# Performance work log

Hardware: AMD Instinct MI355X
Metric: run time of the kernel (lower is better)

The kernel has to match this reference:

```python
import jax, jax.numpy as jnp
import numpy as np
import math

ALPHA = 1.3
N_ITER = 50


def entmax_bisect(logits, alpha=ALPHA, n_iter=N_ITER):
    # logits: [..., D]; entmax over the last axis via bisection on tau.
    x = logits / max(1.0, abs(alpha - 1.0))  # divisor is 1.0 for alpha=1.3
    x = x - jnp.max(x, axis=-1, keepdims=True)  # max_x subtraction (differentiable, as in torch)
    xs = jax.lax.stop_gradient(x)  # tau_lo/tau_hi are .detach()'d in the original
    tau_lo = jnp.min(xs, axis=-1, keepdims=True) - 1.0
    tau_hi = jnp.max(xs, axis=-1, keepdims=True) - 1e-6
    inv = 1.0 / (alpha - 1.0)

    def body(_, carry):
        lo, hi = carry
        tau = (lo + hi) * 0.5
        p = jnp.maximum(xs - tau, 0.0) ** inv
        f = jnp.sum(p, axis=-1, keepdims=True) ** (alpha - 1.0)
        big = f > 1.0
        return (jnp.where(big, tau, lo), jnp.where(big, hi, tau))

    tau_lo, tau_hi = jax.lax.fori_loop(0, n_iter, body, (tau_lo, tau_hi))
    tau = (tau_lo + tau_hi) * 0.5
    p = jnp.maximum(x - tau, 0.0) ** inv
    return p / (jnp.sum(p, axis=-1, keepdims=True) + 1e-12)


def setup_inputs() -> dict:
    key = jax.random.key(0)
    kq, kk, kv = jax.random.split(key, 3)
    B, N, D = 16, 2048, 64
    return {
        "q": jax.random.normal(kq, (B, N, D), dtype=jnp.float32),
        "k": jax.random.normal(kk, (B, N, D), dtype=jnp.float32),
        "v": jax.random.normal(kv, (B, N, D), dtype=jnp.float32),
    }


def reference(q, k, v):
    d = q.shape[-1]
    scores = jnp.einsum("bnd,bmd->bnm", q, k) / math.sqrt(d)  # [B,N,N]
    attn = entmax_bisect(scores, alpha=ALPHA)
    out = jnp.einsum("bnm,bmd->bnd", attn, v)
    return out, attn
```

## Files before the change

### kernel.cpp

```cpp
#include <hip/hip_runtime.h>


#define NBATCH 16
#define NSEQ   2048
#define DHEAD  64
#define OUT_OFF (NBATCH * NSEQ * DHEAD)
#define INV_A    3.3333333f
#define INV_A_M1 2.3333333f

typedef float  vfloat4 __attribute__((ext_vector_type(4)));
typedef float  f32x4   __attribute__((ext_vector_type(4)));
typedef short  bf16x8  __attribute__((ext_vector_type(8)));
typedef unsigned short u16x8 __attribute__((ext_vector_type(8)));

__device__ __forceinline__ float fast_log2(float x) { return __builtin_amdgcn_logf(x); }
__device__ __forceinline__ float fast_exp2(float x) { return __builtin_amdgcn_exp2f(x); }

__device__ __forceinline__ unsigned bf16_rne(float x) {
    const unsigned u = __float_as_uint(x);
    return (u + 0x7FFFu + ((u >> 16) & 1u)) >> 16;
}

__global__ __launch_bounds__(256) void ksplit_kernel(
    const float* __restrict__ K, unsigned short* __restrict__ Khi,
    unsigned short* __restrict__ Klo)
{
    const size_t idx = (size_t)blockIdx.x * 256 + threadIdx.x;
    const float4 x = ((const float4*)K)[idx];
    const float xs[4] = {x.x, x.y, x.z, x.w};
    unsigned short h[4], l[4];
    #pragma unroll
    for (int i = 0; i < 4; ++i) {
        const unsigned hr = bf16_rne(xs[i]);
        h[i] = (unsigned short)hr;
        l[i] = (unsigned short)bf16_rne(xs[i] - __uint_as_float(hr << 16));
    }
    ((ushort4*)Khi)[idx] = make_ushort4(h[0], h[1], h[2], h[3]);
    ((ushort4*)Klo)[idx] = make_ushort4(l[0], l[1], l[2], l[3]);
}

__global__ __launch_bounds__(512, 4) void entmax_attn_kernel(
    const float* __restrict__ Q, const float* __restrict__ V,
    float* __restrict__ Out,
    const unsigned short* __restrict__ Khi, const unsigned short* __restrict__ Klo)
{
    __shared__ __align__(16) float reg0[8192];
    __shared__ __align__(16) float cvx[8 * 512];

    const int tid  = threadIdx.x;
    const int w    = tid >> 6;
    const int lane = tid & 63;
    const int arow = lane & 15;
    const int lg   = lane >> 4;

    const int i   = blockIdx.x;
    const int xcd = i & 7;
    const int j2  = i >> 3;
    const int b   = xcd + 8 * (j2 & 1);
    const int rb  = j2 >> 1;
    const int n0  = rb * 16;

    const float* Vb = V + (size_t)b * NSEQ * DHEAD;
    const unsigned short* KhiB = Khi + (size_t)b * NSEQ * DHEAD;
    const unsigned short* KloB = Klo + (size_t)b * NSEQ * DHEAD;
    char* ldsHi = (char*)reg0;
    char* ldsLo = (char*)reg0 + 16384;

    bf16x8 a_hi[2], a_lo[2];
    {
        const float* qrow = Q + ((size_t)b * NSEQ + (size_t)(n0 + arow)) * DHEAD;
        #pragma unroll
        for (int ks = 0; ks < 2; ++ks) {
            const int d0 = ks * 32 + lg * 8;
            const float4 x0 = *(const float4*)(qrow + d0);
            const float4 x1 = *(const float4*)(qrow + d0 + 4);
            const float xs[8] = {x0.x, x0.y, x0.z, x0.w, x1.x, x1.y, x1.z, x1.w};
            #pragma unroll
            for (int e = 0; e < 8; ++e) {
                const float xq = xs[e] * 0.125f;
                const unsigned hr = bf16_rne(xq);
                a_hi[ks][e] = (short)hr;
                a_lo[ks][e] = (short)bf16_rne(xq - __uint_as_float(hr << 16));
            }
        }
    }

    float s[2][32];
    const int kap = 16 * w + arow;

    const int keyA = tid >> 3, cA = tid & 7;
    const int keyB = keyA + 64;
    const size_t gA = (size_t)keyA * DHEAD + cA * 8;
    const size_t gB = (size_t)keyB * DHEAD + cA * 8;
    const int ofA = keyA * 128 + ((cA ^ (keyA & 7)) << 4);
    const int ofB = keyB * 128 + ((cA ^ (keyA & 7)) << 4);

    u16x8 shA = *(const u16x8*)(KhiB + gA), slA = *(const u16x8*)(KloB + gA);
    u16x8 shB = *(const u16x8*)(KhiB + gB), slB = *(const u16x8*)(KloB + gB);

    #pragma unroll
    for (int g = 0; g < 4; ++g) {
        f32x4 acc[4];
        #pragma unroll
        for (int tt = 0; tt < 4; ++tt) acc[tt] = (f32x4){0.f, 0.f, 0.f, 0.f};

        #pragma unroll
        for (int tt = 0; tt < 4; ++tt) {
            const int t = 4 * g + tt;
            __syncthreads();
            *(u16x8*)(ldsHi + ofA) = shA;  *(u16x8*)(ldsLo + ofA) = slA;
            *(u16x8*)(ldsHi + ofB) = shB;  *(u16x8*)(ldsLo + ofB) = slB;
            __syncthreads();

            #pragma unroll
            for (int ks = 0; ks < 2; ++ks) {
                const int loff = kap * 128 + ((((ks << 2) | lg) ^ (kap & 7)) << 4);
                const bf16x8 bh = *(const bf16x8*)(ldsHi + loff);
                const bf16x8 bl = *(const bf16x8*)(ldsLo + loff);
                acc[tt] = __builtin_amdgcn_mfma_f32_16x16x32_bf16(a_hi[ks], bh, acc[tt], 0, 0, 0);
                acc[tt] = __builtin_amdgcn_mfma_f32_16x16x32_bf16(a_hi[ks], bl, acc[tt], 0, 0, 0);
                acc[tt] = __builtin_amdgcn_mfma_f32_16x16x32_bf16(a_lo[ks], bh, acc[tt], 0, 0, 0);
            }
            if (t < 15) {
                const size_t tb = (size_t)(t + 1) * (128 * DHEAD);
                shA = *(const u16x8*)(KhiB + tb + gA);
                slA = *(const u16x8*)(KloB + tb + gA);
                shB = *(const u16x8*)(KhiB + tb + gB);
                slB = *(const u16x8*)(KloB + tb + gB);
            }
        }

        __syncthreads();
        #pragma unroll
        for (int tt = 0; tt < 4; ++tt)
            #pragma unroll
            for (int i2 = 0; i2 < 4; ++i2)
                reg0[(lg * 4 + i2) * 512 + tt * 128 + kap] = acc[tt][i2];
        __syncthreads();
        #pragma unroll
        for (int r = 0; r < 2; ++r)
            #pragma unroll
            for (int jj = 0; jj < 8; ++jj)
                s[r][8 * g + jj] = reg0[(2 * w + r) * 512 + jj * 64 + lane];
    }
    __syncthreads();

    float* prow  = reg0 + w * 1024;
    float* cval0 = cvx + w * 512;
    float* cidx0 = cval0 + 128;
    float* cval1 = cval0 + 256;
    float* cidx1 = cval0 + 384;
    const unsigned long long lt_mask = (1ull << lane) - 1ull;
    const int na = n0 + 2 * w;

    float mx0 = s[0][0], mx1 = s[1][0];
    #pragma unroll
    for (int j = 1; j < 32; ++j) { mx0 = fmaxf(mx0, s[0][j]); mx1 = fmaxf(mx1, s[1][j]); }
    #pragma unroll
    for (int off = 32; off >= 1; off >>= 1) {
        mx0 = fmaxf(mx0, __shfl_xor(mx0, off, 64));
        mx1 = fmaxf(mx1, __shfl_xor(mx1, off, 64));
    }
    #pragma unroll
    for (int j = 0; j < 32; ++j) { s[0][j] -= mx0; s[1][j] -= mx1; }

    int base0 = 0, base1 = 0;
    #pragma unroll
    for (int j = 0; j < 32; ++j) {
        const bool a0 = s[0][j] > -1.0f;
        const bool a1 = s[1][j] > -1.0f;
        const unsigned long long bm0 = __ballot(a0);
        const unsigned long long bm1 = __ballot(a1);
        const int q0 = base0 + __popcll(bm0 & lt_mask);
        const int q1 = base1 + __popcll(bm1 & lt_mask);
        if (a0 && q0 < 128) { cval0[q0] = s[0][j]; cidx0[q0] = (float)(j * 64 + lane); }
        if (a1 && q1 < 128) { cval1[q1] = s[1][j]; cidx1[q1] = (float)(j * 64 + lane); }
        base0 += __popcll(bm0);
        base1 += __popcll(bm1);
    }
    const int A0 = base0, A1 = base1;

    float* arow0 = Out + OUT_OFF + ((size_t)b * NSEQ + na) * NSEQ;
    float* arow1 = arow0 + NSEQ;

    if (A0 <= 128 && A1 <= 128) {
        const float cv00 = cval0[lane], cv01 = cval0[64 + lane];
        const float cv10 = cval1[lane], cv11 = cval1[64 + lane];
        const bool ok00 = lane < A0, ok01 = 64 + lane < A0;
        const bool ok10 = lane < A1, ok11 = 64 + lane < A1;

        float lo0 = -1.0f, hi0 = -1e-6f, lo1 = -1.0f, hi1 = -1e-6f;
        #pragma unroll 1
        for (int it = 0; it < 12; ++it) {
            const float ta = 0.5f * (lo0 + hi0);
            const float tb = 0.5f * (lo1 + hi1);
            const float t00 = cv00 - ta, t01 = cv01 - ta;
            const float t10 = cv10 - tb, t11 = cv11 - tb;
            float S0 = ((ok00 && t00 > 0.f) ? fast_exp2(INV_A * fast_log2(t00)) : 0.f)
                     + ((ok01 && t01 > 0.f) ? fast_exp2(INV_A * fast_log2(t01)) : 0.f);
            float S1 = ((ok10 && t10 > 0.f) ? fast_exp2(INV_A * fast_log2(t10)) : 0.f)
                     + ((ok11 && t11 > 0.f) ? fast_exp2(INV_A * fast_log2(t11)) : 0.f);
            #pragma unroll
            for (int off = 32; off >= 1; off >>= 1) {
                S0 += __shfl_xor(S0, off, 64);
                S1 += __shfl_xor(S1, off, 64);
            }
            if (S0 > 1.f) lo0 = ta; else hi0 = ta;
            if (S1 > 1.f) lo1 = tb; else hi1 = tb;
        }
        float tau0 = lo0, tau1 = lo1;
        #pragma unroll 1
        for (int it = 0; it < 2; ++it) {
            const float t00 = cv00 - tau0, t01 = cv01 - tau0;
            const float t10 = cv10 - tau1, t11 = cv11 - tau1;
            float Sa0 = 0.f, Sb0 = 0.f, Sa1 = 0.f, Sb1 = 0.f;
            if (ok00 && t00 > 0.f) { const float l = fast_log2(t00); Sa0 += fast_exp2(INV_A * l); Sb0 += fast_exp2(INV_A_M1 * l); }
            if (ok01 && t01 > 0.f) { const float l = fast_log2(t01); Sa0 += fast_exp2(INV_A * l); Sb0 += fast_exp2(INV_A_M1 * l); }
            if (ok10 && t10 > 0.f) { const float l = fast_log2(t10); Sa1 += fast_exp2(INV_A * l); Sb1 += fast_exp2(INV_A_M1 * l); }
            if (ok11 && t11 > 0.f) { const float l = fast_log2(t11); Sa1 += fast_exp2(INV_A * l); Sb1 += fast_exp2(INV_A_M1 * l); }
            #pragma unroll
            for (int off = 32; off >= 1; off >>= 1) {
                Sa0 += __shfl_xor(Sa0, off, 64); Sb0 += __shfl_xor(Sb0, off, 64);
                Sa1 += __shfl_xor(Sa1, off, 64); Sb1 += __shfl_xor(Sb1, off, 64);
            }
            tau0 += (Sa0 - 1.f) / (INV_A * Sb0);
            tau0 = fmaxf(fminf(tau0, hi0), lo0);
            tau1 += (Sa1 - 1.f) / (INV_A * Sb1);
            tau1 = fmaxf(fminf(tau1, hi1), lo1);
        }

        const float t00 = cv00 - tau0, t01 = cv01 - tau0;
        const float t10 = cv10 - tau1, t11 = cv11 - tau1;
        float p00 = (ok00 && t00 > 0.f) ? fast_exp2(INV_A * fast_log2(t00)) : 0.f;
        float p01 = (ok01 && t01 > 0.f) ? fast_exp2(INV_A * fast_log2(t01)) : 0.f;
        float p10 = (ok10 && t10 > 0.f) ? fast_exp2(INV_A * fast_log2(t10)) : 0.f;
        float p11 = (ok11 && t11 > 0.f) ? fast_exp2(INV_A * fast_log2(t11)) : 0.f;
        float S0 = p00 + p01, S1 = p10 + p11;
        #pragma unroll
        for (int off = 32; off >= 1; off >>= 1) {
            S0 += __shfl_xor(S0, off, 64);
            S1 += __shfl_xor(S1, off, 64);
        }
        const float rn0 = 1.f / (S0 + 1e-12f);
        const float rn1 = 1.f / (S1 + 1e-12f);
        p00 *= rn0; p01 *= rn0; p10 *= rn1; p11 *= rn1;
        const int i00 = ok00 ? (int)cidx0[lane] : 0;
        const int i01 = ok01 ? (int)cidx0[64 + lane] : 0;
        const int i10 = ok10 ? (int)cidx1[lane] : 0;
        const int i11 = ok11 ? (int)cidx1[64 + lane] : 0;
        if (ok00) cval0[lane] = p00;
        if (ok01) cval0[64 + lane] = p01;
        if (ok10) cval1[lane] = p10;
        if (ok11) cval1[64 + lane] = p11;

        #pragma unroll
        for (int seg = 0; seg < 2; ++seg) {
            #pragma unroll
            for (int z = 0; z < 4; ++z)
                *(float4*)&prow[(z * 64 + lane) * 4] = make_float4(0.f, 0.f, 0.f, 0.f);
            if (ok00 && (i00 >> 10) == seg) prow[i00 & 1023] = p00;
            if (ok01 && (i01 >> 10) == seg) prow[i01 & 1023] = p01;
            #pragma unroll
            for (int z = 0; z < 4; ++z) {
                const vfloat4 pv = *(const vfloat4*)&prow[(z * 64 + lane) * 4];
                __builtin_nontemporal_store(pv,
                    (vfloat4*)&arow0[seg * 1024 + (z * 64 + lane) * 4]);
            }
        }
        #pragma unroll
        for (int seg = 0; seg < 2; ++seg) {
            #pragma unroll
            for (int z = 0; z < 4; ++z)
                *(float4*)&prow[(z * 64 + lane) * 4] = make_float4(0.f, 0.f, 0.f, 0.f);
            if (ok10 && (i10 >> 10) == seg) prow[i10 & 1023] = p10;
            if (ok11 && (i11 >> 10) == seg) prow[i11 & 1023] = p11;
            #pragma unroll
            for (int z = 0; z < 4; ++z) {
                const vfloat4 pv = *(const vfloat4*)&prow[(z * 64 + lane) * 4];
                __builtin_nontemporal_store(pv,
                    (vfloat4*)&arow1[seg * 1024 + (z * 64 + lane) * 4]);
            }
        }

        float out0 = 0.f, out1 = 0.f;
        int ii = 0;
        #pragma unroll 1
        for (; ii + 8 <= A0; ii += 8) {
            const float pa = cval0[ii+0], pb = cval0[ii+1], pc = cval0[ii+2], pd = cval0[ii+3];
            const float pe = cval0[ii+4], pf = cval0[ii+5], pg = cval0[ii+6], ph = cval0[ii+7];
            const int ma = (int)cidx0[ii+0], mb = (int)cidx0[ii+1], mc = (int)cidx0[ii+2], md = (int)cidx0[ii+3];
            const int me = (int)cidx0[ii+4], mf = (int)cidx0[ii+5], mg = (int)cidx0[ii+6], mh = (int)cidx0[ii+7];
            const float va = Vb[(size_t)ma * DHEAD + lane], vb2 = Vb[(size_t)mb * DHEAD + lane];
            const float vc = Vb[(size_t)mc * DHEAD + lane], vd  = Vb[(size_t)md * DHEAD + lane];
            const float ve = Vb[(size_t)me * DHEAD + lane], vf  = Vb[(size_t)mf * DHEAD + lane];
            const float vg = Vb[(size_t)mg * DHEAD + lane], vh  = Vb[(size_t)mh * DHEAD + lane];
            out0 += pa*va + pb*vb2 + pc*vc + pd*vd + pe*ve + pf*vf + pg*vg + ph*vh;
        }
        #pragma unroll 1
        for (; ii < A0; ++ii)
            out0 += cval0[ii] * Vb[(size_t)(int)cidx0[ii] * DHEAD + lane];

        int jj = 0;
        #pragma unroll 1
        for (; jj + 8 <= A1; jj += 8) {
            const float pa = cval1[jj+0], pb = cval1[jj+1], pc = cval1[jj+2], pd = cval1[jj+3];
            const float pe = cval1[jj+4], pf = cval1[jj+5], pg = cval1[jj+6], ph = cval1[jj+7];
            const int ma = (int)cidx1[jj+0], mb = (int)cidx1[jj+1], mc = (int)cidx1[jj+2], md = (int)cidx1[jj+3];
            const int me = (int)cidx1[jj+4], mf = (int)cidx1[jj+5], mg = (int)cidx1[jj+6], mh = (int)cidx1[jj+7];
            const float va = Vb[(size_t)ma * DHEAD + lane], vb2 = Vb[(size_t)mb * DHEAD + lane];
            const float vc = Vb[(size_t)mc * DHEAD + lane], vd  = Vb[(size_t)md * DHEAD + lane];
            const float ve = Vb[(size_t)me * DHEAD + lane], vf  = Vb[(size_t)mf * DHEAD + lane];
            const float vg = Vb[(size_t)mg * DHEAD + lane], vh  = Vb[(size_t)mh * DHEAD + lane];
            out1 += pa*va + pb*vb2 + pc*vc + pd*vd + pe*ve + pf*vf + pg*vg + ph*vh;
        }
        #pragma unroll 1
        for (; jj < A1; ++jj)
            out1 += cval1[jj] * Vb[(size_t)(int)cidx1[jj] * DHEAD + lane];

        Out[((size_t)b * NSEQ + na) * DHEAD + lane] = out0;
        Out[((size_t)b * NSEQ + na + 1) * DHEAD + lane] = out1;
    } else {
        #pragma unroll
        for (int r = 0; r < 2; ++r) {
            const int A = r ? A1 : A0;
            float* cval = r ? cval1 : cval0;
            float* cidx = r ? cidx1 : cidx0;
            float* arowX = r ? arow1 : arow0;
            float outacc = 0.f;

            if (A <= 128) {
                const float cv0 = cval[lane];
                const float cv1 = cval[64 + lane];
                const bool ok0 = (lane < A);
                const bool ok1 = (64 + lane < A);

                float lo = -1.0f, hi = -1e-6f;
                #pragma unroll 1
                for (int it = 0; it < 12; ++it) {
                    const float tau = 0.5f * (lo + hi);
                    const float t0 = cv0 - tau, t1 = cv1 - tau;
                    float S = ((ok0 && t0 > 0.f) ? fast_exp2(INV_A * fast_log2(t0)) : 0.f)
                            + ((ok1 && t1 > 0.f) ? fast_exp2(INV_A * fast_log2(t1)) : 0.f);
                    #pragma unroll
                    for (int off = 32; off >= 1; off >>= 1) S += __shfl_xor(S, off, 64);
                    if (S > 1.f) lo = tau; else hi = tau;
                }
                float tau = lo;
                #pragma unroll 1
                for (int it = 0; it < 2; ++it) {
                    const float t0 = cv0 - tau, t1 = cv1 - tau;
                    float S1 = 0.f, S2 = 0.f;
                    if (ok0 && t0 > 0.f) {
                        const float l = fast_log2(t0);
                        S1 += fast_exp2(INV_A * l); S2 += fast_exp2(INV_A_M1 * l);
                    }
                    if (ok1 && t1 > 0.f) {
                        const float l = fast_log2(t1);
                        S1 += fast_exp2(INV_A * l); S2 += fast_exp2(INV_A_M1 * l);
                    }
                    #pragma unroll
                    for (int off = 32; off >= 1; off >>= 1) {
                        S1 += __shfl_xor(S1, off, 64);
                        S2 += __shfl_xor(S2, off, 64);
                    }
                    tau += (S1 - 1.f) / (INV_A * S2);
                    tau = fmaxf(fminf(tau, hi), lo);
                }

                const float t0 = cv0 - tau, t1 = cv1 - tau;
                float p0 = (ok0 && t0 > 0.f) ? fast_exp2(INV_A * fast_log2(t0)) : 0.f;
                float p1 = (ok1 && t1 > 0.f) ? fast_exp2(INV_A * fast_log2(t1)) : 0.f;
                float S = p0 + p1;
                #pragma unroll
                for (int off = 32; off >= 1; off >>= 1) S += __shfl_xor(S, off, 64);
                const float rnorm = 1.f / (S + 1e-12f);
                p0 *= rnorm; p1 *= rnorm;
                const int i0 = ok0 ? (int)cidx[lane] : 0;
                const int i1 = ok1 ? (int)cidx[64 + lane] : 0;
                if (ok0) cval[lane] = p0;
                if (ok1) cval[64 + lane] = p1;

                #pragma unroll
                for (int seg = 0; seg < 2; ++seg) {
                    #pragma unroll
                    for (int z = 0; z < 4; ++z)
                        *(float4*)&prow[(z * 64 + lane) * 4] = make_float4(0.f, 0.f, 0.f, 0.f);
                    if (ok0 && (i0 >> 10) == seg) prow[i0 & 1023] = p0;
                    if (ok1 && (i1 >> 10) == seg) prow[i1 & 1023] = p1;
                    #pragma unroll
                    for (int z = 0; z < 4; ++z) {
                        const vfloat4 pv = *(const vfloat4*)&prow[(z * 64 + lane) * 4];
                        __builtin_nontemporal_store(pv,
                            (vfloat4*)&arowX[seg * 1024 + (z * 64 + lane) * 4]);
                    }
                }

                int ii = 0;
                #pragma unroll 1
                for (; ii + 4 <= A; ii += 4) {
                    const float pa = cval[ii + 0], pb = cval[ii + 1];
                    const float pc = cval[ii + 2], pd = cval[ii + 3];
                    const int ma = (int)cidx[ii + 0], mb = (int)cidx[ii + 1];
                    const int mc = (int)cidx[ii + 2], md = (int)cidx[ii + 3];
                    const float va = Vb[(size_t)ma * DHEAD + lane];
                    const float vb2 = Vb[(size_t)mb * DHEAD + lane];
                    const float vc = Vb[(size_t)mc * DHEAD + lane];
                    const float vd = Vb[(size_t)md * DHEAD + lane];
                    outacc += pa * va + pb * vb2 + pc * vc + pd * vd;
                }
                #pragma unroll 1
                for (; ii < A; ++ii)
                    outacc += cval[ii] * Vb[(size_t)(int)cidx[ii] * DHEAD + lane];
            } else {
                float lo = -1.0f, hi = -1e-6f;
                #pragma unroll 1
                for (int it = 0; it < 12; ++it) {
                    const float tau = 0.5f * (lo + hi);
                    float S = 0.f;
                    #pragma unroll
                    for (int j = 0; j < 32; ++j) {
                        const float t = s[r][j] - tau;
                        const float p = fast_exp2(INV_A * fast_log2(t));
                        S += (t > 0.f) ? p : 0.f;
                    }
                    #pragma unroll
                    for (int off = 32; off >= 1; off >>= 1) S += __shfl_xor(S, off, 64);
                    if (S > 1.f) lo = tau; else hi = tau;
                }
                float tau = lo;
                #pragma unroll 1
                for (int it = 0; it < 2; ++it) {
                    float S1 = 0.f, S2 = 0.f;
                    #pragma unroll
                    for (int j = 0; j < 32; ++j) {
                        const float t = s[r][j] - tau;
                        if (t > 0.f) {
                            const float l = fast_log2(t);
                            S1 += fast_exp2(INV_A * l); S2 += fast_exp2(INV_A_M1 * l);
                        }
                    }
                    #pragma unroll
                    for (int off = 32; off >= 1; off >>= 1) {
                        S1 += __shfl_xor(S1, off, 64);
                        S2 += __shfl_xor(S2, off, 64);
                    }
                    tau += (S1 - 1.f) / (INV_A * S2);
                    tau = fmaxf(fminf(tau, hi), lo);
                }
                float S = 0.f;
                #pragma unroll
                for (int j = 0; j < 32; ++j) {
                    const float t = s[r][j] - tau;
                    const float p = (t > 0.f) ? fast_exp2(INV_A * fast_log2(t)) : 0.f;
                    s[r][j] = p;
                    S += p;
                }
                #pragma unroll
                for (int off = 32; off >= 1; off >>= 1) S += __shfl_xor(S, off, 64);
                const float rnorm = 1.f / (S + 1e-12f);

                #pragma unroll
                for (int seg = 0; seg < 2; ++seg) {
                    #pragma unroll
                    for (int jj = 0; jj < 16; ++jj)
                        prow[jj * 64 + lane] = s[r][seg * 16 + jj] * rnorm;
                    #pragma unroll
                    for (int z = 0; z < 16; ++z)
                        __builtin_nontemporal_store(prow[z * 64 + lane],
                                                    &arowX[seg * 1024 + z * 64 + lane]);
                    #pragma unroll 4
                    for (int m = 0; m < 1024; ++m)
                        outacc += prow[m] * Vb[(size_t)(seg * 1024 + m) * DHEAD + lane];
                }
            }

            Out[((size_t)b * NSEQ + (na + r)) * DHEAD + lane] = outacc;
        }
    }
}

extern "C" void kernel_launch(void* const* d_in, const int* in_sizes, int n_in,
                              void* d_out, int out_size, void* d_ws, size_t ws_size,
                              hipStream_t stream) {
    const float* q = (const float*)d_in[0];
    const float* k = (const float*)d_in[1];
    const float* v = (const float*)d_in[2];
    float* out = (float*)d_out;
    (void)in_sizes; (void)n_in; (void)out_size; (void)ws_size;

    unsigned short* Khi = (unsigned short*)d_ws;
    unsigned short* Klo = Khi + (size_t)NBATCH * NSEQ * DHEAD;

    hipLaunchKernelGGL(ksplit_kernel, dim3(2048), dim3(256), 0, stream, k, Khi, Klo);
    hipLaunchKernelGGL(entmax_attn_kernel, dim3(2048), dim3(512), 0, stream,
                       q, v, out, Khi, Klo);
}
```

Before: 451.9 us.

## Pack candidate value and index into one word, cut bisection iterations, recompute dense fallback

Candidate logits and their column indices are packed into a single 32-bit word (value mantissa truncated, index in the low 11 bits), halving the shared-memory candidate buffer and the loads in the sparse gather loops. The number of bisection iterations before the Newton refinement drops from 12 to 8 or 10 on the sparse paths. The rare dense fallback now recomputes scores from fp32 K instead of keeping them live in registers, and uses shuffles instead of shared memory for the P·V product. This lowers register and LDS pressure. The costs are truncated precision on the stored values and probabilities, fewer bisection steps, and removal of the explicit occupancy hint from launch bounds.

Result: slower. 641.0 us (+41.8%).

```diff
diff --git a/kernel.cpp b/kernel.cpp
--- a/kernel.cpp
+++ b/kernel.cpp
@@ -7,6 +7,8 @@
 #define OUT_OFF (NBATCH * NSEQ * DHEAD)
 #define INV_A    3.3333333f
 #define INV_A_M1 2.3333333f
+#define IDXM 0x7FFu
+#define VALM 0xFFFFF800u
 
 typedef float  vfloat4 __attribute__((ext_vector_type(4)));
 typedef float  f32x4   __attribute__((ext_vector_type(4)));
@@ -39,13 +41,13 @@
     ((ushort4*)Klo)[idx] = make_ushort4(l[0], l[1], l[2], l[3]);
 }
 
-__global__ __launch_bounds__(512, 4) void entmax_attn_kernel(
-    const float* __restrict__ Q, const float* __restrict__ V,
-    float* __restrict__ Out,
+__global__ __launch_bounds__(512) void entmax_attn_kernel(
+    const float* __restrict__ Q, const float* __restrict__ K,
+    const float* __restrict__ V, float* __restrict__ Out,
     const unsigned short* __restrict__ Khi, const unsigned short* __restrict__ Klo)
 {
     __shared__ __align__(16) float reg0[8192];
-    __shared__ __align__(16) float cvx[8 * 512];
+    __shared__ __align__(16) float cpk[8 * 256];
 
     const int tid  = threadIdx.x;
     const int w    = tid >> 6;
@@ -60,6 +62,7 @@
     const int rb  = j2 >> 1;
     const int n0  = rb * 16;
 
+    const float* Kb = K + (size_t)b * NSEQ * DHEAD;
     const float* Vb = V + (size_t)b * NSEQ * DHEAD;
     const unsigned short* KhiB = Khi + (size_t)b * NSEQ * DHEAD;
     const unsigned short* KloB = Klo + (size_t)b * NSEQ * DHEAD;
@@ -145,11 +148,9 @@
     }
     __syncthreads();
 
-    float* prow  = reg0 + w * 1024;
-    float* cval0 = cvx + w * 512;
-    float* cidx0 = cval0 + 128;
-    float* cval1 = cval0 + 256;
-    float* cidx1 = cval0 + 384;
+    unsigned* pk0 = (unsigned*)(cpk + w * 256);
+    unsigned* pk1 = pk0 + 128;
+    float* prow = reg0 + w * 1024;
     const unsigned long long lt_mask = (1ull << lane) - 1ull;
     const int na = n0 + 2 * w;
 
@@ -161,20 +162,21 @@
         mx0 = fmaxf(mx0, __shfl_xor(mx0, off, 64));
         mx1 = fmaxf(mx1, __shfl_xor(mx1, off, 64));
     }
-    #pragma unroll
-    for (int j = 0; j < 32; ++j) { s[0][j] -= mx0; s[1][j] -= mx1; }
 
     int base0 = 0, base1 = 0;
     #pragma unroll
     for (int j = 0; j < 32; ++j) {
-        const bool a0 = s[0][j] > -1.0f;
-        const bool a1 = s[1][j] > -1.0f;
+        const float v0 = s[0][j] - mx0;
+        const float v1 = s[1][j] - mx1;
+        const bool a0 = v0 > -1.0f;
+        const bool a1 = v1 > -1.0f;
         const unsigned long long bm0 = __ballot(a0);
         const unsigned long long bm1 = __ballot(a1);
         const int q0 = base0 + __popcll(bm0 & lt_mask);
         const int q1 = base1 + __popcll(bm1 & lt_mask);
-        if (a0 && q0 < 128) { cval0[q0] = s[0][j]; cidx0[q0] = (float)(j * 64 + lane); }
-        if (a1 && q1 < 128) { cval1[q1] = s[1][j]; cidx1[q1] = (float)(j * 64 + lane); }
+        const unsigned idx = (unsigned)(j * 64 + lane);
+        if (a0 && q0 < 128) pk0[q0] = (__float_as_uint(v0) & VALM) | idx;
+        if (a1 && q1 < 128) pk1[q1] = (__float_as_uint(v1) & VALM) | idx;
         base0 += __popcll(bm0);
         base1 += __popcll(bm1);
     }
@@ -184,14 +186,18 @@
     float* arow1 = arow0 + NSEQ;
 
     if (A0 <= 128 && A1 <= 128) {
-        const float cv00 = cval0[lane], cv01 = cval0[64 + lane];
-        const float cv10 = cval1[lane], cv11 = cval1[64 + lane];
+        const unsigned u00 = pk0[lane],      u01 = pk0[64 + lane];
+        const unsigned u10 = pk1[lane],      u11 = pk1[64 + lane];
+        const float cv00 = __uint_as_float(u00 & VALM);
+        const float cv01 = __uint_as_float(u01 & VALM);
+        const float cv10 = __uint_as_float(u10 & VALM);
+        const float cv11 = __uint_as_float(u11 & VALM);
         const bool ok00 = lane < A0, ok01 = 64 + lane < A0;
         const bool ok10 = lane < A1, ok11 = 64 + lane < A1;
 
         float lo0 = -1.0f, hi0 = -1e-6f, lo1 = -1.0f, hi1 = -1e-6f;
         #pragma unroll 1
-        for (int it = 0; it < 12; ++it) {
+        for (int it = 0; it < 8; ++it) {
             const float ta = 0.5f * (lo0 + hi0);
             const float tb = 0.5f * (lo1 + hi1);
             const float t00 = cv00 - ta, t01 = cv01 - ta;
@@ -244,14 +250,14 @@
         const float rn0 = 1.f / (S0 + 1e-12f);
         const float rn1 = 1.f / (S1 + 1e-12f);
         p00 *= rn0; p01 *= rn0; p10 *= rn1; p11 *= rn1;
-        const int i00 = ok00 ? (int)cidx0[lane] : 0;
-        const int i01 = ok01 ? (int)cidx0[64 + lane] : 0;
-        const int i10 = ok10 ? (int)cidx1[lane] : 0;
-        const int i11 = ok11 ? (int)cidx1[64 + lane] : 0;
-        if (ok00) cval0[lane] = p00;
-        if (ok01) cval0[64 + lane] = p01;
-        if (ok10) cval1[lane] = p10;
-        if (ok11) cval1[64 + lane] = p11;
+        const int i00 = ok00 ? (int)(u00 & IDXM) : -1;
+        const int i01 = ok01 ? (int)(u01 & IDXM) : -1;
+        const int i10 = ok10 ? (int)(u10 & IDXM) : -1;
+        const int i11 = ok11 ? (int)(u11 & IDXM) : -1;
+        if (ok00) pk0[lane]      = (__float_as_uint(p00) & VALM) | (unsigned)i00;
+        if (ok01) pk0[64 + lane] = (__float_as_uint(p01) & VALM) | (unsigned)i01;
+        if (ok10) pk1[lane]      = (__float_as_uint(p10) & VALM) | (unsigned)i10;
+        if (ok11) pk1[64 + lane] = (__float_as_uint(p11) & VALM) | (unsigned)i11;
 
         #pragma unroll
         for (int seg = 0; seg < 2; ++seg) {
@@ -286,57 +292,62 @@
         int ii = 0;
         #pragma unroll 1
         for (; ii + 8 <= A0; ii += 8) {
-            const float pa = cval0[ii+0], pb = cval0[ii+1], pc = cval0[ii+2], pd = cval0[ii+3];
-            const float pe = cval0[ii+4], pf = cval0[ii+5], pg = cval0[ii+6], ph = cval0[ii+7];
-            const int ma = (int)cidx0[ii+0], mb = (int)cidx0[ii+1], mc = (int)cidx0[ii+2], md = (int)cidx0[ii+3];
-            const int me = (int)cidx0[ii+4], mf = (int)cidx0[ii+5], mg = (int)cidx0[ii+6], mh = (int)cidx0[ii+7];
-            const float va = Vb[(size_t)ma * DHEAD + lane], vb2 = Vb[(size_t)mb * DHEAD + lane];
-            const float vc = Vb[(size_t)mc * DHEAD + lane], vd  = Vb[(size_t)md * DHEAD + lane];
-            const float ve = Vb[(size_t)me * DHEAD + lane], vf  = Vb[(size_t)mf * DHEAD + lane];
-            const float vg = Vb[(size_t)mg * DHEAD + lane], vh  = Vb[(size_t)mh * DHEAD + lane];
-            out0 += pa*va + pb*vb2 + pc*vc + pd*vd + pe*ve + pf*vf + pg*vg + ph*vh;
-        }
-        #pragma unroll 1
-        for (; ii < A0; ++ii)
-            out0 += cval0[ii] * Vb[(size_t)(int)cidx0[ii] * DHEAD + lane];
-
+            const unsigned ua = pk0[ii+0], ub = pk0[ii+1], uc = pk0[ii+2], ud = pk0[ii+3];
+            const unsigned ue = pk0[ii+4], uf = pk0[ii+5], ug = pk0[ii+6], uh = pk0[ii+7];
+            out0 += __uint_as_float(ua & VALM) * Vb[(size_t)(ua & IDXM) * DHEAD + lane]
+                  + __uint_as_float(ub & VALM) * Vb[(size_t)(ub & IDXM) * DHEAD + lane]
+                  + __uint_as_float(uc & VALM) * Vb[(size_t)(uc & IDXM) * DHEAD + lane]
+                  + __uint_as_float(ud & VALM) * Vb[(size_t)(ud & IDXM) * DHEAD + lane]
+                  + __uint_as_float(ue & VALM) * Vb[(size_t)(ue & IDXM) * DHEAD + lane]
+                  + __uint_as_float(uf & VALM) * Vb[(size_t)(uf & IDXM) * DHEAD + lane]
+                  + __uint_as_float(ug & VALM) * Vb[(size_t)(ug & IDXM) * DHEAD + lane]
+                  + __uint_as_float(uh & VALM) * Vb[(size_t)(uh & IDXM) * DHEAD + lane];
+        }
+        #pragma unroll 1
+        for (; ii < A0; ++ii) {
+            const unsigned ua = pk0[ii];
+            out0 += __uint_as_float(ua & VALM) * Vb[(size_t)(ua & IDXM) * DHEAD + lane];
+        }
         int jj = 0;
         #pragma unroll 1
         for (; jj + 8 <= A1; jj += 8) {
-            const float pa = cval1[jj+0], pb = cval1[jj+1], pc = cval1[jj+2], pd = cval1[jj+3];
-            const float pe = cval1[jj+4], pf = cval1[jj+5], pg = cval1[jj+6], ph = cval1[jj+7];
-            const int ma = (int)cidx1[jj+0], mb = (int)cidx1[jj+1], mc = (int)cidx1[jj+2], md = (int)cidx1[jj+3];
-            const int me = (int)cidx1[jj+4], mf = (int)cidx1[jj+5], mg = (int)cidx1[jj+6], mh = (int)cidx1[jj+7];
-            const float va = Vb[(size_t)ma * DHEAD + lane], vb2 = Vb[(size_t)mb * DHEAD + lane];
-            const float vc = Vb[(size_t)mc * DHEAD + lane], vd  = Vb[(size_t)md * DHEAD + lane];
-            const float ve = Vb[(size_t)me * DHEAD + lane], vf  = Vb[(size_t)mf * DHEAD + lane];
-            const float vg = Vb[(size_t)mg * DHEAD + lane], vh  = Vb[(size_t)mh * DHEAD + lane];
-            out1 += pa*va + pb*vb2 + pc*vc + pd*vd + pe*ve + pf*vf + pg*vg + ph*vh;
-        }
-        #pragma unroll 1
-        for (; jj < A1; ++jj)
-            out1 += cval1[jj] * Vb[(size_t)(int)cidx1[jj] * DHEAD + lane];
+            const unsigned ua = pk1[jj+0], ub = pk1[jj+1], uc = pk1[jj+2], ud = pk1[jj+3];
+            const unsigned ue = pk1[jj+4], uf = pk1[jj+5], ug = pk1[jj+6], uh = pk1[jj+7];
+            out1 += __uint_as_float(ua & VALM) * Vb[(size_t)(ua & IDXM) * DHEAD + lane]
+                  + __uint_as_float(ub & VALM) * Vb[(size_t)(ub & IDXM) * DHEAD + lane]
+                  + __uint_as_float(uc & VALM) * Vb[(size_t)(uc & IDXM) * DHEAD + lane]
+                  + __uint_as_float(ud & VALM) * Vb[(size_t)(ud & IDXM) * DHEAD + lane]
+                  + __uint_as_float(ue & VALM) * Vb[(size_t)(ue & IDXM) * DHEAD + lane]
+                  + __uint_as_float(uf & VALM) * Vb[(size_t)(uf & IDXM) * DHEAD + lane]
+                  + __uint_as_float(ug & VALM) * Vb[(size_t)(ug & IDXM) * DHEAD + lane]
+                  + __uint_as_float(uh & VALM) * Vb[(size_t)(uh & IDXM) * DHEAD + lane];
+        }
+        #pragma unroll 1
+        for (; jj < A1; ++jj) {
+            const unsigned ua = pk1[jj];
+            out1 += __uint_as_float(ua & VALM) * Vb[(size_t)(ua & IDXM) * DHEAD + lane];
+        }
 
         Out[((size_t)b * NSEQ + na) * DHEAD + lane] = out0;
         Out[((size_t)b * NSEQ + na + 1) * DHEAD + lane] = out1;
     } else {
-        #pragma unroll
+        #pragma unroll 1
         for (int r = 0; r < 2; ++r) {
             const int A = r ? A1 : A0;
-            float* cval = r ? cval1 : cval0;
-            float* cidx = r ? cidx1 : cidx0;
+            unsigned* pk = r ? pk1 : pk0;
             float* arowX = r ? arow1 : arow0;
             float outacc = 0.f;
 
             if (A <= 128) {
-                const float cv0 = cval[lane];
-                const float cv1 = cval[64 + lane];
+                const unsigned u0 = pk[lane], u1 = pk[64 + lane];
+                const float cv0 = __uint_as_float(u0 & VALM);
+                const float cv1 = __uint_as_float(u1 & VALM);
                 const bool ok0 = (lane < A);
                 const bool ok1 = (64 + lane < A);
 
                 float lo = -1.0f, hi = -1e-6f;
                 #pragma unroll 1
-                for (int it = 0; it < 12; ++it) {
+                for (int it = 0; it < 10; ++it) {
                     const float tau = 0.5f * (lo + hi);
                     const float t0 = cv0 - tau, t1 = cv1 - tau;
                     float S = ((ok0 && t0 > 0.f) ? fast_exp2(INV_A * fast_log2(t0)) : 0.f)
@@ -350,14 +361,8 @@
                 for (int it = 0; it < 2; ++it) {
                     const float t0 = cv0 - tau, t1 = cv1 - tau;
                     float S1 = 0.f, S2 = 0.f;
-                    if (ok0 && t0 > 0.f) {
-                        const float l = fast_log2(t0);
-                        S1 += fast_exp2(INV_A * l); S2 += fast_exp2(INV_A_M1 * l);
-                    }
-                    if (ok1 && t1 > 0.f) {
-                        const float l = fast_log2(t1);
-                        S1 += fast_exp2(INV_A * l); S2 += fast_exp2(INV_A_M1 * l);
-                    }
+                    if (ok0 && t0 > 0.f) { const float l = fast_log2(t0); S1 += fast_exp2(INV_A * l); S2 += fast_exp2(INV_A_M1 * l); }
+                    if (ok1 && t1 > 0.f) { const float l = fast_log2(t1); S1 += fast_exp2(INV_A * l); S2 += fast_exp2(INV_A_M1 * l); }
                     #pragma unroll
                     for (int off = 32; off >= 1; off >>= 1) {
                         S1 += __shfl_xor(S1, off, 64);
@@ -366,7 +371,6 @@
                     tau += (S1 - 1.f) / (INV_A * S2);
                     tau = fmaxf(fminf(tau, hi), lo);
                 }
-
                 const float t0 = cv0 - tau, t1 = cv1 - tau;
                 float p0 = (ok0 && t0 > 0.f) ? fast_exp2(INV_A * fast_log2(t0)) : 0.f;
                 float p1 = (ok1 && t1 > 0.f) ? fast_exp2(INV_A * fast_log2(t1)) : 0.f;
@@ -375,10 +379,10 @@
                 for (int off = 32; off >= 1; off >>= 1) S += __shfl_xor(S, off, 64);
                 const float rnorm = 1.f / (S + 1e-12f);
                 p0 *= rnorm; p1 *= rnorm;
-                const int i0 = ok0 ? (int)cidx[lane] : 0;
-                const int i1 = ok1 ? (int)cidx[64 + lane] : 0;
-                if (ok0) cval[lane] = p0;
-                if (ok1) cval[64 + lane] = p1;
+                const int i0 = ok0 ? (int)(u0 & IDXM) : -1;
+                const int i1 = ok1 ? (int)(u1 & IDXM) : -1;
+                if (ok0) pk[lane]      = (__float_as_uint(p0) & VALM) | (unsigned)i0;
+                if (ok1) pk[64 + lane] = (__float_as_uint(p1) & VALM) | (unsigned)i1;
 
                 #pragma unroll
                 for (int seg = 0; seg < 2; ++seg) {
@@ -398,20 +402,40 @@
                 int ii = 0;
                 #pragma unroll 1
                 for (; ii + 4 <= A; ii += 4) {
-                    const float pa = cval[ii + 0], pb = cval[ii + 1];
-                    const float pc = cval[ii + 2], pd = cval[ii + 3];
-                    const int ma = (int)cidx[ii + 0], mb = (int)cidx[ii + 1];
-                    const int mc = (int)cidx[ii + 2], md = (int)cidx[ii + 3];
-                    const float va = Vb[(size_t)ma * DHEAD + lane];
-                    const float vb2 = Vb[(size_t)mb * DHEAD + lane];
-                    const float vc = Vb[(size_t)mc * DHEAD + lane];
-                    const float vd = Vb[(size_t)md * DHEAD + lane];
-                    outacc += pa * va + pb * vb2 + pc * vc + pd * vd;
-                }
-                #pragma unroll 1
-                for (; ii < A; ++ii)
-                    outacc += cval[ii] * Vb[(size_t)(int)cidx[ii] * DHEAD + lane];
+                    const unsigned ua = pk[ii+0], ub = pk[ii+1], uc = pk[ii+2], ud = pk[ii+3];
+                    outacc += __uint_as_float(ua & VALM) * Vb[(size_t)(ua & IDXM) * DHEAD + lane]
+                            + __uint_as_float(ub & VALM) * Vb[(size_t)(ub & IDXM) * DHEAD + lane]
+                            + __uint_as_float(uc & VALM) * Vb[(size_t)(uc & IDXM) * DHEAD + lane]
+                            + __uint_as_float(ud & VALM) * Vb[(size_t)(ud & IDXM) * DHEAD + lane];
+                }
+                #pragma unroll 1
+                for (; ii < A; ++ii) {
+                    const unsigned ua = pk[ii];
+                    outacc += __uint_as_float(ua & VALM) * Vb[(size_t)(ua & IDXM) * DHEAD + lane];
+                }
             } else {
+                const float* qr = Q + ((size_t)b * NSEQ + (size_t)(na + r)) * DHEAD;
+                float xd[32];
+                #pragma unroll 1
+                for (int j = 0; j < 32; ++j) {
+                    const float* kr = Kb + (size_t)(j * 64 + lane) * DHEAD;
+                    float d = 0.f;
+                    #pragma unroll
+                    for (int c = 0; c < 16; ++c) {
+                        const float4 qa = ((const float4*)qr)[c];
+                        const float4 ka = ((const float4*)kr)[c];
+                        d += qa.x*ka.x + qa.y*ka.y + qa.z*ka.z + qa.w*ka.w;
+                    }
+                    xd[j] = d * 0.125f;
+                }
+                float mxe = xd[0];
+                #pragma unroll
+                for (int j = 1; j < 32; ++j) mxe = fmaxf(mxe, xd[j]);
+                #pragma unroll
+                for (int off = 32; off >= 1; off >>= 1) mxe = fmaxf(mxe, __shfl_xor(mxe, off, 64));
+                #pragma unroll
+                for (int j = 0; j < 32; ++j) xd[j] -= mxe;
+
                 float lo = -1.0f, hi = -1e-6f;
                 #pragma unroll 1
                 for (int it = 0; it < 12; ++it) {
@@ -419,7 +443,7 @@
                     float S = 0.f;
                     #pragma unroll
                     for (int j = 0; j < 32; ++j) {
-                        const float t = s[r][j] - tau;
+                        const float t = xd[j] - tau;
                         const float p = fast_exp2(INV_A * fast_log2(t));
                         S += (t > 0.f) ? p : 0.f;
                     }
@@ -433,7 +457,7 @@
                     float S1 = 0.f, S2 = 0.f;
                     #pragma unroll
                     for (int j = 0; j < 32; ++j) {
-                        const float t = s[r][j] - tau;
+                        const float t = xd[j] - tau;
                         if (t > 0.f) {
                             const float l = fast_log2(t);
                             S1 += fast_exp2(INV_A * l); S2 += fast_exp2(INV_A_M1 * l);
@@ -448,29 +472,29 @@
                     tau = fmaxf(fminf(tau, hi), lo);
                 }
                 float S = 0.f;
+                float pd[32];
                 #pragma unroll
                 for (int j = 0; j < 32; ++j) {
-                    const float t = s[r][j] - tau;
+                    const float t = xd[j] - tau;
                     const float p = (t > 0.f) ? fast_exp2(INV_A * fast_log2(t)) : 0.f;
-                    s[r][j] = p;
+                    pd[j] = p;
                     S += p;
                 }
                 #pragma unroll
                 for (int off = 32; off >= 1; off >>= 1) S += __shfl_xor(S, off, 64);
                 const float rnorm = 1.f / (S + 1e-12f);
-
-                #pragma unroll
-                for (int seg = 0; seg < 2; ++seg) {
-                    #pragma unroll
-                    for (int jj = 0; jj < 16; ++jj)
-                        prow[jj * 64 + lane] = s[r][seg * 16 + jj] * rnorm;
-                    #pragma unroll
-                    for (int z = 0; z < 16; ++z)
-                        __builtin_nontemporal_store(prow[z * 64 + lane],
-                                                    &arowX[seg * 1024 + z * 64 + lane]);
-                    #pragma unroll 4
-                    for (int m = 0; m < 1024; ++m)
-                        outacc += prow[m] * Vb[(size_t)(seg * 1024 + m) * DHEAD + lane];
+                #pragma unroll
+                for (int j = 0; j < 32; ++j) {
+                    pd[j] *= rnorm;
+                    __builtin_nontemporal_store(pd[j], &arowX[j * 64 + lane]);
+                }
+                #pragma unroll 1
+                for (int j = 0; j < 32; ++j) {
+                    #pragma unroll 1
+                    for (int l = 0; l < 64; ++l) {
+                        const float pv = __shfl(pd[j], l, 64);
+                        outacc += pv * Vb[(size_t)(j * 64 + l) * DHEAD + lane];
+                    }
                 }
             }
 
@@ -493,5 +517,5 @@
 
     hipLaunchKernelGGL(ksplit_kernel, dim3(2048), dim3(256), 0, stream, k, Khi, Klo);
     hipLaunchKernelGGL(entmax_attn_kernel, dim3(2048), dim3(512), 0, stream,
-                       q, v, out, Khi, Klo);
+                       q, k, v, out, Khi, Klo);
 }
```
